# Performance work log

Measured on AMD Instinct MI355X. Metric: run time of the kernel, lower is better.

## Reference

```python
import jax, jax.numpy as jnp
import numpy as np

EPS = 1e-5  # nn.LayerNorm default eps


def setup_inputs() -> dict:
    key = jax.random.key(0)
    k1, k2, k3, k4 = jax.random.split(key, 4)
    B, S, HS, N = 4, 8192, 1024, 4
    x = jax.random.normal(k1, (B, S, HS), dtype=jnp.float32)
    alpha = jax.random.uniform(k2, (B, S, N), dtype=jnp.float32)
    W = jax.random.normal(k3, (N, HS), dtype=jnp.float32)
    b = jax.random.normal(k4, (N, HS), dtype=jnp.float32)
    return {"x": x, "alpha": alpha, "W": W, "b": b}


def reference(x, alpha, W, b):
    # All anchors normalize the same x, so compute the normalization once.
    mean = jnp.mean(x, axis=-1, keepdims=True)
    var = jnp.mean(jnp.square(x - mean), axis=-1, keepdims=True)  # biased, as in torch LayerNorm
    xhat = (x - mean) * jax.lax.rsqrt(var + EPS)  # [B, S, HS]
    # alpha-weighted mixture of per-anchor affine params:
    # out = sum_n alpha_n * (xhat * W_n + b_n) = xhat * (alpha @ W) + (alpha @ b)
    eff_w = jnp.einsum('bsn,nh->bsh', alpha, W)
    eff_b = jnp.einsum('bsn,nh->bsh', alpha, b)
    return xhat * eff_w + eff_b
```

## Files before the change

kernel.cpp:

```cpp
#include <hip/hip_runtime.h>


constexpr int HS = 1024;

__global__ __launch_bounds__(256, 2) void lns_kernel(
    const float* __restrict__ x,
    const float* __restrict__ alpha,
    const float* __restrict__ W,
    const float* __restrict__ Bias,
    float* __restrict__ out,
    int nrows)
{
    const int t = threadIdx.x;
    const int h4 = t * 4;

    const float4 w0 = *reinterpret_cast<const float4*>(W + 0 * HS + h4);
    const float4 w1 = *reinterpret_cast<const float4*>(W + 1 * HS + h4);
    const float4 w2 = *reinterpret_cast<const float4*>(W + 2 * HS + h4);
    const float4 w3 = *reinterpret_cast<const float4*>(W + 3 * HS + h4);
    const float4 b0 = *reinterpret_cast<const float4*>(Bias + 0 * HS + h4);
    const float4 b1 = *reinterpret_cast<const float4*>(Bias + 1 * HS + h4);
    const float4 b2 = *reinterpret_cast<const float4*>(Bias + 2 * HS + h4);
    const float4 b3 = *reinterpret_cast<const float4*>(Bias + 3 * HS + h4);

    __shared__ float red[8];

    for (int row = blockIdx.x; row < nrows; row += gridDim.x) {
        const size_t base = (size_t)row * HS + h4;
        const float4 xv = *reinterpret_cast<const float4*>(x + base);

        float s  = (xv.x + xv.y) + (xv.z + xv.w);
        float ss = fmaf(xv.x, xv.x, fmaf(xv.y, xv.y, fmaf(xv.z, xv.z, xv.w * xv.w)));

        #pragma unroll
        for (int off = 32; off > 0; off >>= 1) {
            s  += __shfl_down(s, off, 64);
            ss += __shfl_down(ss, off, 64);
        }
        const int wv = t >> 6;
        if ((t & 63) == 0) { red[wv] = s; red[wv + 4] = ss; }
        __syncthreads();
        s  = (red[0] + red[1]) + (red[2] + red[3]);
        ss = (red[4] + red[5]) + (red[6] + red[7]);
        __syncthreads();

        const float mean = s * (1.0f / HS);
        const float var  = fmaf(-mean, mean, ss * (1.0f / HS));
        const float rstd = rsqrtf(var + 1e-5f);

        const float4 av = *reinterpret_cast<const float4*>(alpha + (size_t)row * 4);

        float4 o;
        {
            const float ew = fmaf(av.x, w0.x, fmaf(av.y, w1.x, fmaf(av.z, w2.x, av.w * w3.x)));
            const float eb = fmaf(av.x, b0.x, fmaf(av.y, b1.x, fmaf(av.z, b2.x, av.w * b3.x)));
            o.x = fmaf((xv.x - mean) * rstd, ew, eb);
        }
        {
            const float ew = fmaf(av.x, w0.y, fmaf(av.y, w1.y, fmaf(av.z, w2.y, av.w * w3.y)));
            const float eb = fmaf(av.x, b0.y, fmaf(av.y, b1.y, fmaf(av.z, b2.y, av.w * b3.y)));
            o.y = fmaf((xv.y - mean) * rstd, ew, eb);
        }
        {
            const float ew = fmaf(av.x, w0.z, fmaf(av.y, w1.z, fmaf(av.z, w2.z, av.w * w3.z)));
            const float eb = fmaf(av.x, b0.z, fmaf(av.y, b1.z, fmaf(av.z, b2.z, av.w * b3.z)));
            o.z = fmaf((xv.z - mean) * rstd, ew, eb);
        }
        {
            const float ew = fmaf(av.x, w0.w, fmaf(av.y, w1.w, fmaf(av.z, w2.w, av.w * w3.w)));
            const float eb = fmaf(av.x, b0.w, fmaf(av.y, b1.w, fmaf(av.z, b2.w, av.w * b3.w)));
            o.w = fmaf((xv.w - mean) * rstd, ew, eb);
        }

        *reinterpret_cast<float4*>(out + base) = o;
    }
}

extern "C" void kernel_launch(void* const* d_in, const int* in_sizes, int n_in,
                              void* d_out, int out_size, void* d_ws, size_t ws_size,
                              hipStream_t stream) {
    const float* x     = (const float*)d_in[0];
    const float* alpha = (const float*)d_in[1];
    const float* W     = (const float*)d_in[2];
    const float* Bias  = (const float*)d_in[3];
    float* out = (float*)d_out;

    const int nrows = in_sizes[0] / HS;

    const int grid = 2048;
    lns_kernel<<<grid, 256, 0, stream>>>(x, alpha, W, Bias, out, nrows);
}
```

Before: 49.14 us.

## Process two rows per iteration with double-buffered reduction and nontemporal stores

Each block now handles two rows per loop iteration, issuing both x loads up front to raise memory-level parallelism. The block reduction uses a double-buffered shared array, which drops one of the two barriers per iteration. Output is written with nontemporal stores to avoid polluting cache, and launch bounds now request higher occupancy. Register pressure rises, and the grid of 2048 now covers 4096 rows per pass, so each block runs fewer iterations.

```diff
diff --git a/kernel.cpp b/kernel.cpp
--- a/kernel.cpp
+++ b/kernel.cpp
@@ -3,7 +3,18 @@
 
 constexpr int HS = 1024;
 
-__global__ __launch_bounds__(256, 2) void lns_kernel(
+typedef float vfloat4 __attribute__((ext_vector_type(4)));
+
+__device__ __forceinline__ float4 ld4(const float* p) {
+    return *reinterpret_cast<const float4*>(p);
+}
+
+__device__ __forceinline__ void st4_nt(float* p, float a, float b, float c, float d) {
+    vfloat4 v = {a, b, c, d};
+    __builtin_nontemporal_store(v, reinterpret_cast<vfloat4*>(p));
+}
+
+__global__ __launch_bounds__(256, 8) void lns_kernel(
     const float* __restrict__ x,
     const float* __restrict__ alpha,
     const float* __restrict__ W,
@@ -14,65 +25,95 @@
     const int t = threadIdx.x;
     const int h4 = t * 4;
 
-    const float4 w0 = *reinterpret_cast<const float4*>(W + 0 * HS + h4);
-    const float4 w1 = *reinterpret_cast<const float4*>(W + 1 * HS + h4);
-    const float4 w2 = *reinterpret_cast<const float4*>(W + 2 * HS + h4);
-    const float4 w3 = *reinterpret_cast<const float4*>(W + 3 * HS + h4);
-    const float4 b0 = *reinterpret_cast<const float4*>(Bias + 0 * HS + h4);
-    const float4 b1 = *reinterpret_cast<const float4*>(Bias + 1 * HS + h4);
-    const float4 b2 = *reinterpret_cast<const float4*>(Bias + 2 * HS + h4);
-    const float4 b3 = *reinterpret_cast<const float4*>(Bias + 3 * HS + h4);
+    const float4 w0 = ld4(W + 0 * HS + h4);
+    const float4 w1 = ld4(W + 1 * HS + h4);
+    const float4 w2 = ld4(W + 2 * HS + h4);
+    const float4 w3 = ld4(W + 3 * HS + h4);
+    const float4 b0 = ld4(Bias + 0 * HS + h4);
+    const float4 b1 = ld4(Bias + 1 * HS + h4);
+    const float4 b2 = ld4(Bias + 2 * HS + h4);
+    const float4 b3 = ld4(Bias + 3 * HS + h4);
 
-    __shared__ float red[8];
+    __shared__ float red[2][16];
 
-    for (int row = blockIdx.x; row < nrows; row += gridDim.x) {
-        const size_t base = (size_t)row * HS + h4;
-        const float4 xv = *reinterpret_cast<const float4*>(x + base);
+    const int wv = t >> 6;
+    int iter = 0;
 
-        float s  = (xv.x + xv.y) + (xv.z + xv.w);
-        float ss = fmaf(xv.x, xv.x, fmaf(xv.y, xv.y, fmaf(xv.z, xv.z, xv.w * xv.w)));
+    for (int row = blockIdx.x * 2; row < nrows; row += gridDim.x * 2, ++iter) {
+        const size_t base0 = (size_t)row * HS + h4;
+        const size_t base1 = base0 + HS;
+
+        const float4 x0 = ld4(x + base0);
+        const float4 x1 = ld4(x + base1);
+        const float4 a0 = ld4(alpha + (size_t)row * 4);
+        const float4 a1 = ld4(alpha + (size_t)row * 4 + 4);
+
+        float s0  = (x0.x + x0.y) + (x0.z + x0.w);
+        float ss0 = fmaf(x0.x, x0.x, fmaf(x0.y, x0.y, fmaf(x0.z, x0.z, x0.w * x0.w)));
+        float s1  = (x1.x + x1.y) + (x1.z + x1.w);
+        float ss1 = fmaf(x1.x, x1.x, fmaf(x1.y, x1.y, fmaf(x1.z, x1.z, x1.w * x1.w)));
 
         #pragma unroll
         for (int off = 32; off > 0; off >>= 1) {
-            s  += __shfl_down(s, off, 64);
-            ss += __shfl_down(ss, off, 64);
+            s0  += __shfl_down(s0,  off, 64);
+            ss0 += __shfl_down(ss0, off, 64);
+            s1  += __shfl_down(s1,  off, 64);
+            ss1 += __shfl_down(ss1, off, 64);
         }
-        const int wv = t >> 6;
-        if ((t & 63) == 0) { red[wv] = s; red[wv + 4] = ss; }
-        __syncthreads();
-        s  = (red[0] + red[1]) + (red[2] + red[3]);
-        ss = (red[4] + red[5]) + (red[6] + red[7]);
+
+        const int p = iter & 1;
+        if ((t & 63) == 0) {
+            red[p][wv]      = s0;
+            red[p][4 + wv]  = ss0;
+            red[p][8 + wv]  = s1;
+            red[p][12 + wv] = ss1;
+        }
         __syncthreads();
 
-        const float mean = s * (1.0f / HS);
-        const float var  = fmaf(-mean, mean, ss * (1.0f / HS));
-        const float rstd = rsqrtf(var + 1e-5f);
+        s0  = (red[p][0] + red[p][1]) + (red[p][2] + red[p][3]);
+        ss0 = (red[p][4] + red[p][5]) + (red[p][6] + red[p][7]);
+        s1  = (red[p][8] + red[p][9]) + (red[p][10] + red[p][11]);
+        ss1 = (red[p][12] + red[p][13]) + (red[p][14] + red[p][15]);
 
-        const float4 av = *reinterpret_cast<const float4*>(alpha + (size_t)row * 4);
+        const float mean0 = s0 * (1.0f / HS);
+        const float var0  = fmaf(-mean0, mean0, ss0 * (1.0f / HS));
+        const float rstd0 = rsqrtf(var0 + 1e-5f);
+        const float mean1 = s1 * (1.0f / HS);
+        const float var1  = fmaf(-mean1, mean1, ss1 * (1.0f / HS));
+        const float rstd1 = rsqrtf(var1 + 1e-5f);
 
-        float4 o;
+        float o0x, o0y, o0z, o0w, o1x, o1y, o1z, o1w;
         {
-            const float ew = fmaf(av.x, w0.x, fmaf(av.y, w1.x, fmaf(av.z, w2.x, av.w * w3.x)));
-            const float eb = fmaf(av.x, b0.x, fmaf(av.y, b1.x, fmaf(av.z, b2.x, av.w * b3.x)));
-            o.x = fmaf((xv.x - mean) * rstd, ew, eb);
-        }
-        {
-            const float ew = fmaf(av.x, w0.y, fmaf(av.y, w1.y, fmaf(av.z, w2.y, av.w * w3.y)));
-            const float eb = fmaf(av.x, b0.y, fmaf(av.y, b1.y, fmaf(av.z, b2.y, av.w * b3.y)));
-            o.y = fmaf((xv.y - mean) * rstd, ew, eb);
-        }
-        {
-            const float ew = fmaf(av.x, w0.z, fmaf(av.y, w1.z, fmaf(av.z, w2.z, av.w * w3.z)));
-            const float eb = fmaf(av.x, b0.z, fmaf(av.y, b1.z, fmaf(av.z, b2.z, av.w * b3.z)));
-            o.z = fmaf((xv.z - mean) * rstd, ew, eb);
-        }
-        {
-            const float ew = fmaf(av.x, w0.w, fmaf(av.y, w1.w, fmaf(av.z, w2.w, av.w * w3.w)));
-            const float eb = fmaf(av.x, b0.w, fmaf(av.y, b1.w, fmaf(av.z, b2.w, av.w * b3.w)));
-            o.w = fmaf((xv.w - mean) * rstd, ew, eb);
+            float ew, eb;
+            ew = fmaf(a0.x, w0.x, fmaf(a0.y, w1.x, fmaf(a0.z, w2.x, a0.w * w3.x)));
+            eb = fmaf(a0.x, b0.x, fmaf(a0.y, b1.x, fmaf(a0.z, b2.x, a0.w * b3.x)));
+            o0x = fmaf((x0.x - mean0) * rstd0, ew, eb);
+            ew = fmaf(a0.x, w0.y, fmaf(a0.y, w1.y, fmaf(a0.z, w2.y, a0.w * w3.y)));
+            eb = fmaf(a0.x, b0.y, fmaf(a0.y, b1.y, fmaf(a0.z, b2.y, a0.w * b3.y)));
+            o0y = fmaf((x0.y - mean0) * rstd0, ew, eb);
+            ew = fmaf(a0.x, w0.z, fmaf(a0.y, w1.z, fmaf(a0.z, w2.z, a0.w * w3.z)));
+            eb = fmaf(a0.x, b0.z, fmaf(a0.y, b1.z, fmaf(a0.z, b2.z, a0.w * b3.z)));
+            o0z = fmaf((x0.z - mean0) * rstd0, ew, eb);
+            ew = fmaf(a0.x, w0.w, fmaf(a0.y, w1.w, fmaf(a0.z, w2.w, a0.w * w3.w)));
+            eb = fmaf(a0.x, b0.w, fmaf(a0.y, b1.w, fmaf(a0.z, b2.w, a0.w * b3.w)));
+            o0w = fmaf((x0.w - mean0) * rstd0, ew, eb);
+
+            ew = fmaf(a1.x, w0.x, fmaf(a1.y, w1.x, fmaf(a1.z, w2.x, a1.w * w3.x)));
+            eb = fmaf(a1.x, b0.x, fmaf(a1.y, b1.x, fmaf(a1.z, b2.x, a1.w * b3.x)));
+            o1x = fmaf((x1.x - mean1) * rstd1, ew, eb);
+            ew = fmaf(a1.x, w0.y, fmaf(a1.y, w1.y, fmaf(a1.z, w2.y, a1.w * w3.y)));
+            eb = fmaf(a1.x, b0.y, fmaf(a1.y, b1.y, fmaf(a1.z, b2.y, a1.w * b3.y)));
+            o1y = fmaf((x1.y - mean1) * rstd1, ew, eb);
+            ew = fmaf(a1.x, w0.z, fmaf(a1.y, w1.z, fmaf(a1.z, w2.z, a1.w * w3.z)));
+            eb = fmaf(a1.x, b0.z, fmaf(a1.y, b1.z, fmaf(a1.z, b2.z, a1.w * b3.z)));
+            o1z = fmaf((x1.z - mean1) * rstd1, ew, eb);
+            ew = fmaf(a1.x, w0.w, fmaf(a1.y, w1.w, fmaf(a1.z, w2.w, a1.w * w3.w)));
+            eb = fmaf(a1.x, b0.w, fmaf(a1.y, b1.w, fmaf(a1.z, b2.w, a1.w * b3.w)));
+            o1w = fmaf((x1.w - mean1) * rstd1, ew, eb);
         }
 
-        *reinterpret_cast<float4*>(out + base) = o;
+        st4_nt(out + base0, o0x, o0y, o0z, o0w);
+        st4_nt(out + base1, o1x, o1y, o1z, o1w);
     }
 }
 
```

Measured after the change: 47.29 us. 1.04x faster.
